# Kernel tuning notes

Measured on AMD Instinct MI355X. Metric: run time of the kernel, lower is better.

Reference implementation:

```python
import jax, jax.numpy as jnp
import numpy as np

NUM_FEATURES = 10000
EMBED_DIM = 64
BATCH = 16384


def setup_inputs() -> dict:
    key = jax.random.key(0)
    k1, k2 = jax.random.split(key)
    # binary multi-hot indicator matrix [B, F]
    multi_hot = jax.random.randint(k1, (BATCH, NUM_FEATURES), 0, 2, dtype=jnp.int32)
    # xavier_uniform init: bound = sqrt(6 / (fan_in + fan_out))
    bound = float(np.sqrt(6.0 / (NUM_FEATURES + EMBED_DIM)))
    embed_matrix = jax.random.uniform(
        k2, (NUM_FEATURES, EMBED_DIM), minval=-bound, maxval=bound, dtype=jnp.float32
    )
    return {"multi_hot": multi_hot, "embed_matrix": embed_matrix}


def reference(multi_hot, embed_matrix):
    # multi_hot.float() @ embed_matrix  -> [B, D]
    return jnp.matmul(multi_hot.astype(embed_matrix.dtype), embed_matrix)
```

## Files before the change

kernel.cpp:

```cpp
#include <hip/hip_runtime.h>


typedef int    int4v   __attribute__((ext_vector_type(4)));
typedef float  float4v __attribute__((ext_vector_type(4)));
typedef float  f32x4   __attribute__((ext_vector_type(4)));
typedef short  bf16x8  __attribute__((ext_vector_type(8)));
typedef unsigned int uint4v __attribute__((ext_vector_type(4)));

constexpr int M_DIM   = 16384;
constexpr int K_DIM   = 10000;
constexpr int N_DIM   = 64;
constexpr int BK      = 64;
constexpr int NCH_PAD = 160;
constexpr int KPAD    = NCH_PAD * BK;
constexpr int SPLIT   = 4;
constexpr int NCH_SEG = NCH_PAD / SPLIT;
constexpr int WM      = 32;

__device__ __forceinline__ unsigned f2bf(float x) {
    unsigned u = __builtin_bit_cast(unsigned, x);
    u += 0x7FFFu + ((u >> 16) & 1u);
    return u >> 16;
}

__global__ __launch_bounds__(256) void prep(const float* __restrict__ em,
                                            unsigned short* __restrict__ bt,
                                            float* __restrict__ out) {
    const int tid = threadIdx.x;
    const int b   = blockIdx.x;
    if (b < NCH_PAD) {
        __shared__ float t[64][65];
        const int k0 = b * 64;
        #pragma unroll
        for (int rep = 0; rep < 16; ++rep) {
            const int idx = rep * 256 + tid;
            const int k = idx >> 6, n = idx & 63;
            float v = 0.f;
            if (k0 + k < K_DIM) v = em[(k0 + k) * N_DIM + n];
            t[n][k] = v;
        }
        __syncthreads();
        const int n  = tid >> 2;
        const int kk = (tid & 3) * 16;
        unsigned w[8];
        #pragma unroll
        for (int j = 0; j < 8; ++j)
            w[j] = f2bf(t[n][kk + 2 * j]) | (f2bf(t[n][kk + 2 * j + 1]) << 16);
        uint4v lo = {w[0], w[1], w[2], w[3]};
        uint4v hi = {w[4], w[5], w[6], w[7]};
        uint4v* dst = (uint4v*)(bt + (long long)n * KPAD + k0 + kk);
        dst[0] = lo; dst[1] = hi;
    } else {
        const int b2 = b - NCH_PAD;
        float4v z = {0.f, 0.f, 0.f, 0.f};
        float4v* p = (float4v*)out;
        const int base = b2 * 256 + tid;
        #pragma unroll
        for (int i = 0; i < 4; ++i) p[base + i * 65536] = z;
    }
}

struct ARegs { int4v q0, q1, q2, q3; };
struct BF    { bf16x8 f[4][2]; };

__global__ __launch_bounds__(256, 2) void mhe_gemm(
        const int* __restrict__ mh, const unsigned short* __restrict__ bt,
        float* __restrict__ out) {
    const int tid  = threadIdx.x;
    const int lane = tid & 63;
    const int wv   = tid >> 6;
    const int w    = (int)blockIdx.x * 4 + wv;
    const int seg  = w >> 9;
    const int rowblk = w & 511;
    const int row0 = rowblk * WM;
    const int c0   = seg * NCH_SEG;

    const int g8 = (lane >> 4) << 3;
    const int* __restrict__ ap0 = mh + (long long)(row0 + (lane & 15)) * K_DIM;
    const int* __restrict__ ap1 = ap0 + (long long)16 * K_DIM;

    const unsigned short* __restrict__ bpn[4];
    #pragma unroll
    for (int nt = 0; nt < 4; ++nt)
        bpn[nt] = bt + (long long)(nt * 16 + (lane & 15)) * KPAD + g8;

    f32x4 acc[2][4] = {};

    auto packA = [&](int4v qa, int4v qb) -> bf16x8 {
        uint4v x;
        x[0] = (unsigned)(qa[0] | (qa[1] << 16)) * 0x3F80u;
        x[1] = (unsigned)(qa[2] | (qa[3] << 16)) * 0x3F80u;
        x[2] = (unsigned)(qb[0] | (qb[1] << 16)) * 0x3F80u;
        x[3] = (unsigned)(qb[2] | (qb[3] << 16)) * 0x3F80u;
        return __builtin_bit_cast(bf16x8, x);
    };

    auto loadAB = [&](ARegs& x0, ARegs& x1, BF& bb, int c) {
        const int f0 = c * BK;
        if (f0 + BK <= K_DIM) {
            const int4v* p0 = (const int4v*)(ap0 + f0 + g8);
            const int4v* p1 = (const int4v*)(ap0 + f0 + 32 + g8);
            const int4v* p2 = (const int4v*)(ap1 + f0 + g8);
            const int4v* p3 = (const int4v*)(ap1 + f0 + 32 + g8);
            x0.q0 = __builtin_nontemporal_load(p0);
            x0.q1 = __builtin_nontemporal_load(p0 + 1);
            x0.q2 = __builtin_nontemporal_load(p1);
            x0.q3 = __builtin_nontemporal_load(p1 + 1);
            x1.q0 = __builtin_nontemporal_load(p2);
            x1.q1 = __builtin_nontemporal_load(p2 + 1);
            x1.q2 = __builtin_nontemporal_load(p3);
            x1.q3 = __builtin_nontemporal_load(p3 + 1);
        } else {
            x0.q0 = {}; x0.q1 = {}; x0.q2 = {}; x0.q3 = {};
            x1.q0 = {}; x1.q1 = {}; x1.q2 = {}; x1.q3 = {};
            const int b0 = f0 + g8;
            if (b0      < K_DIM) { x0.q0 = *(const int4v*)(ap0 + b0);
                                   x1.q0 = *(const int4v*)(ap1 + b0); }
            if (b0 + 4  < K_DIM) { x0.q1 = *(const int4v*)(ap0 + b0 + 4);
                                   x1.q1 = *(const int4v*)(ap1 + b0 + 4); }
            if (b0 + 32 < K_DIM) { x0.q2 = *(const int4v*)(ap0 + b0 + 32);
                                   x1.q2 = *(const int4v*)(ap1 + b0 + 32); }
            if (b0 + 36 < K_DIM) { x0.q3 = *(const int4v*)(ap0 + b0 + 36);
                                   x1.q3 = *(const int4v*)(ap1 + b0 + 36); }
        }
        #pragma unroll
        for (int nt = 0; nt < 4; ++nt) {
            bb.f[nt][0] = *(const bf16x8*)(bpn[nt] + f0);
            bb.f[nt][1] = *(const bf16x8*)(bpn[nt] + f0 + 32);
        }
    };

    auto compute = [&](const ARegs& x0, const ARegs& x1, const BF& bb) {
        bf16x8 a00 = packA(x0.q0, x0.q1);
        bf16x8 a01 = packA(x0.q2, x0.q3);
        bf16x8 a10 = packA(x1.q0, x1.q1);
        bf16x8 a11 = packA(x1.q2, x1.q3);
        #pragma unroll
        for (int nt = 0; nt < 4; ++nt) {
            acc[0][nt] = __builtin_amdgcn_mfma_f32_16x16x32_bf16(a00, bb.f[nt][0], acc[0][nt], 0, 0, 0);
            acc[0][nt] = __builtin_amdgcn_mfma_f32_16x16x32_bf16(a01, bb.f[nt][1], acc[0][nt], 0, 0, 0);
            acc[1][nt] = __builtin_amdgcn_mfma_f32_16x16x32_bf16(a10, bb.f[nt][0], acc[1][nt], 0, 0, 0);
            acc[1][nt] = __builtin_amdgcn_mfma_f32_16x16x32_bf16(a11, bb.f[nt][1], acc[1][nt], 0, 0, 0);
        }
    };

    ARegs a0A, a1A, a0B, a1B;
    BF bA, bB;
    loadAB(a0A, a1A, bA, c0);
    int c = c0;
    for (; c + 2 < c0 + NCH_SEG; c += 2) {
        loadAB(a0B, a1B, bB, c + 1);
        compute(a0A, a1A, bA);
        loadAB(a0A, a1A, bA, c + 2);
        compute(a0B, a1B, bB);
    }
    loadAB(a0B, a1B, bB, c + 1);
    compute(a0A, a1A, bA);
    compute(a0B, a1B, bB);

    const int crow = row0 + ((lane >> 4) << 2);
    const int ccol = lane & 15;
    #pragma unroll
    for (int mt = 0; mt < 2; ++mt)
        #pragma unroll
        for (int nt = 0; nt < 4; ++nt)
            #pragma unroll
            for (int i = 0; i < 4; ++i)
                unsafeAtomicAdd(&out[(long long)(crow + mt * 16 + i) * N_DIM + nt * 16 + ccol],
                                acc[mt][nt][i]);
}

extern "C" void kernel_launch(void* const* d_in, const int* in_sizes, int n_in,
                              void* d_out, int out_size, void* d_ws, size_t ws_size,
                              hipStream_t stream) {
    const int*   mh  = (const int*)d_in[0];
    const float* em  = (const float*)d_in[1];
    float*       out = (float*)d_out;
    unsigned short* bt = (unsigned short*)d_ws;
    (void)in_sizes; (void)n_in; (void)out_size; (void)ws_size;

    prep<<<dim3(NCH_PAD + 256), dim3(256), 0, stream>>>(em, bt, out);
    mhe_gemm<<<dim3((M_DIM / WM) * SPLIT / 4), dim3(256), 0, stream>>>(mh, bt, out);
}
```

Before: 235.6 us.

## Use 16-row wave tiles with 256-wide K superchunks and two-way K split

Each wave now handles 16 rows instead of 32 and covers half of K instead of a quarter. It processes 256-wide K superchunks, issuing four A chunk loads up front for more memory-level parallelism. The ragged K tail is handled by a dedicated block in the second segment, replacing the per-chunk bounds checks. The aim is more bytes of A in flight and fewer output atomics. In exchange, B fragment reuse across row tiles is lost and B register traffic per row roughly doubles.

```diff
diff --git a/kernel.cpp b/kernel.cpp
--- a/kernel.cpp
+++ b/kernel.cpp
@@ -10,12 +10,11 @@
 constexpr int M_DIM   = 16384;
 constexpr int K_DIM   = 10000;
 constexpr int N_DIM   = 64;
-constexpr int BK      = 64;
 constexpr int NCH_PAD = 160;
-constexpr int KPAD    = NCH_PAD * BK;
-constexpr int SPLIT   = 4;
-constexpr int NCH_SEG = NCH_PAD / SPLIT;
-constexpr int WM      = 32;
+constexpr int KPAD    = NCH_PAD * 64;
+constexpr int SPLIT   = 2;
+constexpr int NSC_SEG = 20;
+constexpr int WMR     = 16;
 
 __device__ __forceinline__ unsigned f2bf(float x) {
     unsigned u = __builtin_bit_cast(unsigned, x);
@@ -60,8 +59,8 @@
     }
 }
 
-struct ARegs { int4v q0, q1, q2, q3; };
-struct BF    { bf16x8 f[4][2]; };
+struct AR { int4v  q0, q1, q2, q3; };
+struct BF { bf16x8 f[4][2]; };
 
 __global__ __launch_bounds__(256, 2) void mhe_gemm(
         const int* __restrict__ mh, const unsigned short* __restrict__ bt,
@@ -70,21 +69,19 @@
     const int lane = tid & 63;
     const int wv   = tid >> 6;
     const int w    = (int)blockIdx.x * 4 + wv;
-    const int seg  = w >> 9;
-    const int rowblk = w & 511;
-    const int row0 = rowblk * WM;
-    const int c0   = seg * NCH_SEG;
+    const int seg  = w >> 10;
+    const int rowblk = w & 1023;
+    const int row0 = rowblk * WMR;
 
     const int g8 = (lane >> 4) << 3;
-    const int* __restrict__ ap0 = mh + (long long)(row0 + (lane & 15)) * K_DIM;
-    const int* __restrict__ ap1 = ap0 + (long long)16 * K_DIM;
+    const int* __restrict__ ap = mh + (long long)(row0 + (lane & 15)) * K_DIM;
 
     const unsigned short* __restrict__ bpn[4];
     #pragma unroll
     for (int nt = 0; nt < 4; ++nt)
         bpn[nt] = bt + (long long)(nt * 16 + (lane & 15)) * KPAD + g8;
 
-    f32x4 acc[2][4] = {};
+    f32x4 acc[4] = {};
 
     auto packA = [&](int4v qa, int4v qb) -> bf16x8 {
         uint4v x;
@@ -95,79 +92,68 @@
         return __builtin_bit_cast(bf16x8, x);
     };
 
-    auto loadAB = [&](ARegs& x0, ARegs& x1, BF& bb, int c) {
-        const int f0 = c * BK;
-        if (f0 + BK <= K_DIM) {
-            const int4v* p0 = (const int4v*)(ap0 + f0 + g8);
-            const int4v* p1 = (const int4v*)(ap0 + f0 + 32 + g8);
-            const int4v* p2 = (const int4v*)(ap1 + f0 + g8);
-            const int4v* p3 = (const int4v*)(ap1 + f0 + 32 + g8);
-            x0.q0 = __builtin_nontemporal_load(p0);
-            x0.q1 = __builtin_nontemporal_load(p0 + 1);
-            x0.q2 = __builtin_nontemporal_load(p1);
-            x0.q3 = __builtin_nontemporal_load(p1 + 1);
-            x1.q0 = __builtin_nontemporal_load(p2);
-            x1.q1 = __builtin_nontemporal_load(p2 + 1);
-            x1.q2 = __builtin_nontemporal_load(p3);
-            x1.q3 = __builtin_nontemporal_load(p3 + 1);
-        } else {
-            x0.q0 = {}; x0.q1 = {}; x0.q2 = {}; x0.q3 = {};
-            x1.q0 = {}; x1.q1 = {}; x1.q2 = {}; x1.q3 = {};
-            const int b0 = f0 + g8;
-            if (b0      < K_DIM) { x0.q0 = *(const int4v*)(ap0 + b0);
-                                   x1.q0 = *(const int4v*)(ap1 + b0); }
-            if (b0 + 4  < K_DIM) { x0.q1 = *(const int4v*)(ap0 + b0 + 4);
-                                   x1.q1 = *(const int4v*)(ap1 + b0 + 4); }
-            if (b0 + 32 < K_DIM) { x0.q2 = *(const int4v*)(ap0 + b0 + 32);
-                                   x1.q2 = *(const int4v*)(ap1 + b0 + 32); }
-            if (b0 + 36 < K_DIM) { x0.q3 = *(const int4v*)(ap0 + b0 + 36);
-                                   x1.q3 = *(const int4v*)(ap1 + b0 + 36); }
-        }
+    auto loadA = [&](AR& a, int f0) {
+        a.q0 = __builtin_nontemporal_load((const int4v*)(ap + f0 + g8));
+        a.q1 = __builtin_nontemporal_load((const int4v*)(ap + f0 + g8 + 4));
+        a.q2 = __builtin_nontemporal_load((const int4v*)(ap + f0 + 32 + g8));
+        a.q3 = __builtin_nontemporal_load((const int4v*)(ap + f0 + 32 + g8 + 4));
+    };
+
+    auto loadB = [&](BF& b, int f0) {
         #pragma unroll
         for (int nt = 0; nt < 4; ++nt) {
-            bb.f[nt][0] = *(const bf16x8*)(bpn[nt] + f0);
-            bb.f[nt][1] = *(const bf16x8*)(bpn[nt] + f0 + 32);
+            b.f[nt][0] = *(const bf16x8*)(bpn[nt] + f0);
+            b.f[nt][1] = *(const bf16x8*)(bpn[nt] + f0 + 32);
         }
     };
 
-    auto compute = [&](const ARegs& x0, const ARegs& x1, const BF& bb) {
-        bf16x8 a00 = packA(x0.q0, x0.q1);
-        bf16x8 a01 = packA(x0.q2, x0.q3);
-        bf16x8 a10 = packA(x1.q0, x1.q1);
-        bf16x8 a11 = packA(x1.q2, x1.q3);
+    auto computeChunk = [&](const AR& a, const BF& b) {
+        bf16x8 a0 = packA(a.q0, a.q1);
+        bf16x8 a1 = packA(a.q2, a.q3);
         #pragma unroll
         for (int nt = 0; nt < 4; ++nt) {
-            acc[0][nt] = __builtin_amdgcn_mfma_f32_16x16x32_bf16(a00, bb.f[nt][0], acc[0][nt], 0, 0, 0);
-            acc[0][nt] = __builtin_amdgcn_mfma_f32_16x16x32_bf16(a01, bb.f[nt][1], acc[0][nt], 0, 0, 0);
-            acc[1][nt] = __builtin_amdgcn_mfma_f32_16x16x32_bf16(a10, bb.f[nt][0], acc[1][nt], 0, 0, 0);
-            acc[1][nt] = __builtin_amdgcn_mfma_f32_16x16x32_bf16(a11, bb.f[nt][1], acc[1][nt], 0, 0, 0);
+            acc[nt] = __builtin_amdgcn_mfma_f32_16x16x32_bf16(a0, b.f[nt][0], acc[nt], 0, 0, 0);
+            acc[nt] = __builtin_amdgcn_mfma_f32_16x16x32_bf16(a1, b.f[nt][1], acc[nt], 0, 0, 0);
         }
     };
 
-    ARegs a0A, a1A, a0B, a1B;
-    BF bA, bB;
-    loadAB(a0A, a1A, bA, c0);
-    int c = c0;
-    for (; c + 2 < c0 + NCH_SEG; c += 2) {
-        loadAB(a0B, a1B, bB, c + 1);
-        compute(a0A, a1A, bA);
-        loadAB(a0A, a1A, bA, c + 2);
-        compute(a0B, a1B, bB);
+    const int sc0   = seg * NSC_SEG;
+    const int nfull = NSC_SEG - seg;
+    for (int s = 0; s < nfull; ++s) {
+        const int F = (sc0 + s) * 256;
+        BF b01[2];
+        loadB(b01[0], F);
+        loadB(b01[1], F + 64);
+        AR a[4];
+        #pragma unroll
+        for (int cc = 0; cc < 4; ++cc) loadA(a[cc], F + cc * 64);
+        computeChunk(a[0], b01[0]);
+        computeChunk(a[1], b01[1]);
+        BF b23[2];
+        loadB(b23[0], F + 128);
+        loadB(b23[1], F + 192);
+        computeChunk(a[2], b23[0]);
+        computeChunk(a[3], b23[1]);
     }
-    loadAB(a0B, a1B, bB, c + 1);
-    compute(a0A, a1A, bA);
-    compute(a0B, a1B, bB);
+
+    if (seg == 1) {
+        const int f0 = 9984;
+        AR a; a.q0 = {}; a.q1 = {}; a.q2 = {}; a.q3 = {};
+        if (f0 + g8 + 4 <= K_DIM) a.q0 = *(const int4v*)(ap + f0 + g8);
+        if (f0 + g8 + 8 <= K_DIM) a.q1 = *(const int4v*)(ap + f0 + g8 + 4);
+        BF b;
+        loadB(b, f0);
+        computeChunk(a, b);
+    }
 
     const int crow = row0 + ((lane >> 4) << 2);
     const int ccol = lane & 15;
     #pragma unroll
-    for (int mt = 0; mt < 2; ++mt)
+    for (int nt = 0; nt < 4; ++nt)
         #pragma unroll
-        for (int nt = 0; nt < 4; ++nt)
-            #pragma unroll
-            for (int i = 0; i < 4; ++i)
-                unsafeAtomicAdd(&out[(long long)(crow + mt * 16 + i) * N_DIM + nt * 16 + ccol],
-                                acc[mt][nt][i]);
+        for (int i = 0; i < 4; ++i)
+            unsafeAtomicAdd(&out[(long long)(crow + i) * N_DIM + nt * 16 + ccol],
+                            acc[nt][i]);
 }
 
 extern "C" void kernel_launch(void* const* d_in, const int* in_sizes, int n_in,
@@ -180,5 +166,5 @@
     (void)in_sizes; (void)n_in; (void)out_size; (void)ws_size;
 
     prep<<<dim3(NCH_PAD + 256), dim3(256), 0, stream>>>(em, bt, out);
-    mhe_gemm<<<dim3((M_DIM / WM) * SPLIT / 4), dim3(256), 0, stream>>>(mh, bt, out);
+    mhe_gemm<<<dim3((M_DIM / WMR) * SPLIT / 4), dim3(256), 0, stream>>>(mh, bt, out);
 }
```

Measured after the change: 326.4 us. 38.5% more time.
